# Optimization experiments

Measured on AMD Instinct MI355X. Metric: run time of the kernel, lower is better.

Reference implementation:

```python
import jax, jax.numpy as jnp
import numpy as np

B, S, D_ENC, D_DEC, UNITS = 64, 2048, 512, 512, 512


def setup_inputs() -> dict:
    key = jax.random.key(0)
    ks = jax.random.split(key, 8)
    enc = jax.random.normal(ks[0], (B, S, D_ENC), dtype=jnp.float32)
    dec = jax.random.normal(ks[1], (B, D_DEC), dtype=jnp.float32)
    # Dense params (glorot-ish scale)
    W1 = jax.random.normal(ks[2], (D_ENC, UNITS), dtype=jnp.float32) / np.sqrt(D_ENC)
    b1 = jnp.zeros((UNITS,), dtype=jnp.float32)
    W2 = jax.random.normal(ks[3], (D_DEC, UNITS), dtype=jnp.float32) / np.sqrt(D_DEC)
    b2 = jnp.zeros((UNITS,), dtype=jnp.float32)
    V = jax.random.normal(ks[4], (UNITS, 1), dtype=jnp.float32) / np.sqrt(UNITS)
    bv = jnp.zeros((1,), dtype=jnp.float32)
    return {"encoder_outputs": enc, "decoder_hidden": dec,
            "W1": W1, "b1": b1, "W2": W2, "b2": b2, "V": V, "bv": bv}


def reference(encoder_outputs, decoder_hidden, W1, b1, W2, b2, V, bv):
    # score_features: [B,S,U] = tanh(W1(enc) + W2(dec)[:,None,:])
    proj_enc = jnp.einsum('bsd,du->bsu', encoder_outputs, W1) + b1
    proj_dec = decoder_hidden @ W2 + b2                      # [B,U]
    feat = jnp.tanh(proj_enc + proj_dec[:, None, :])         # [B,S,U]
    score = jnp.einsum('bsu,uo->bso', feat, V) + bv          # [B,S,1]
    attn = jax.nn.softmax(score, axis=1)                     # softmax over seq
    context = jnp.sum(attn * encoder_outputs, axis=1)        # [B,D_enc]
    return context, jnp.squeeze(attn, axis=-1)
```

## Files before the change

kernel.cpp:

```cpp
#include <hip/hip_runtime.h>
#include <hip/hip_bf16.h>

#define BATCH 64
#define SEQ   2048
#define DIM   512
#define MROWS (BATCH * SEQ)

typedef short bf16x8 __attribute__((ext_vector_type(8)));
typedef float f32x4  __attribute__((ext_vector_type(4)));

static __device__ __forceinline__ unsigned short f2bf(float f) {
    union { float f; unsigned u; } v; v.f = f;
    unsigned u = v.u;
    u += 0x7FFFu + ((u >> 16) & 1u);
    return (unsigned short)(u >> 16);
}

static __device__ __forceinline__ float tanh_fast(float x) {
    float xc = fminf(20.0f, fmaxf(-20.0f, x));
#if __has_builtin(__builtin_amdgcn_exp2f)
    float t = __builtin_amdgcn_exp2f(2.885390082f * xc);
#else
    float t = exp2f(2.885390082f * xc);
#endif
#if __has_builtin(__builtin_amdgcn_rcpf)
    return (t - 1.0f) * __builtin_amdgcn_rcpf(t + 1.0f);
#else
    return (t - 1.0f) / (t + 1.0f);
#endif
}

typedef __attribute__((address_space(1))) const unsigned int gu32;
typedef __attribute__((address_space(3))) unsigned int lu32;
static __device__ __forceinline__ void gload_lds16(const unsigned short* g,
                                                   unsigned short* l) {
    __builtin_amdgcn_global_load_lds((gu32*)g, (lu32*)l, 16, 0, 0);
}

__global__ void prep_w1t_kernel(const float* __restrict__ W1,
                                unsigned short* __restrict__ w1t) {
    int stride = gridDim.x * blockDim.x;
    for (int i = blockIdx.x * blockDim.x + threadIdx.x; i < DIM * DIM; i += stride) {
        int k = i >> 9;
        int u = i & 511;
        w1t[u * DIM + k] = f2bf(W1[i]);
    }
}

__global__ void proj_dec_v2(const float* __restrict__ dec,
                            const float* __restrict__ W2,
                            const float* __restrict__ b1,
                            const float* __restrict__ b2,
                            float* __restrict__ pd) {
    __shared__ float sdec[DIM];
    __shared__ float red[4 * 64];
    const int ug = blockIdx.x;
    const int b  = blockIdx.y;
    const int t  = threadIdx.x;
    sdec[t]       = dec[b * DIM + t];
    sdec[t + 256] = dec[b * DIM + t + 256];
    __syncthreads();
    const int u  = ug * 64 + (t & 63);
    const int kq = t >> 6;
    float acc = 0.f;
    #pragma unroll 4
    for (int k = kq * 128; k < kq * 128 + 128; ++k)
        acc += sdec[k] * W2[k * DIM + u];
    red[kq * 64 + (t & 63)] = acc;
    __syncthreads();
    if (t < 64) {
        int u_g = ug * 64 + t;
        float s = red[t] + red[64 + t] + red[128 + t] + red[192 + t]
                + b1[u_g] + b2[u_g];
        pd[b * DIM + u_g] = s;
    }
}

#define BM3 64
#define BK3 64

__global__ __launch_bounds__(256, 2) void gemm_score_v6(
    const float* __restrict__ enc,
    const unsigned short* __restrict__ w1t,
    const float* __restrict__ pd,
    const float* __restrict__ V,
    float* __restrict__ scores,
    float* __restrict__ cnum,
    float* __restrict__ zacc)
{
    __shared__ unsigned short sA[BM3 * BK3];
    __shared__ unsigned short sB[DIM * BK3];

    const int tid  = threadIdx.x;
    const int lane = tid & 63;
    const int wave = tid >> 6;
    const int quad = lane >> 4;
    const int l15  = lane & 15;

    const int row0 = blockIdx.x * BM3;

    f32x4 acc[8][4];
    for (int j = 0; j < 8; ++j)
        for (int tr = 0; tr < 4; ++tr)
            acc[j][tr] = (f32x4){0.f, 0.f, 0.f, 0.f};

    for (int k0 = 0; k0 < DIM; k0 += BK3) {
        for (int i = 0; i < 16; ++i) {
            int c  = i * 256 + tid;
            int r  = c >> 3;
            int cc = c & 7;
            int gc = cc ^ (r & 7);
            gload_lds16(w1t + (size_t)r * DIM + k0 + gc * 8, &sB[c * 8]);
        }
        for (int i = 0; i < 2; ++i) {
            int c  = i * 256 + tid;
            int r  = c >> 3;
            int cc = c & 7;
            const float4* p =
                (const float4*)(enc + (size_t)(row0 + r) * DIM + k0 + cc * 8);
            float4 va = p[0], vb = p[1];
            union { ushort4 s[2]; uint4 q; } o;
            o.s[0].x = f2bf(va.x); o.s[0].y = f2bf(va.y);
            o.s[0].z = f2bf(va.z); o.s[0].w = f2bf(va.w);
            o.s[1].x = f2bf(vb.x); o.s[1].y = f2bf(vb.y);
            o.s[1].z = f2bf(vb.z); o.s[1].w = f2bf(vb.w);
            *(uint4*)(&sA[r * BK3 + ((cc ^ (r & 7)) * 8)]) = o.q;
        }
        __syncthreads();

        for (int kk = 0; kk < BK3; kk += 32) {
            int jc = (kk >> 3) + quad;
            bf16x8 af[4];
            for (int tr = 0; tr < 4; ++tr) {
                int am = tr * 16 + l15;
                af[tr] = *(const bf16x8*)(&sA[am * BK3 + ((jc ^ (am & 7)) * 8)]);
            }
            for (int j = 0; j < 8; ++j) {
                int u = wave * 128 + j * 16 + l15;
                bf16x8 bfr = *(const bf16x8*)(&sB[u * BK3 + ((jc ^ (u & 7)) * 8)]);
                for (int tr = 0; tr < 4; ++tr)
                    acc[j][tr] = __builtin_amdgcn_mfma_f32_16x16x32_bf16(
                        af[tr], bfr, acc[j][tr], 0, 0, 0);
            }
        }
        __syncthreads();
    }

    const int b = row0 >> 11;
    float sacc[4][4];
    for (int tr = 0; tr < 4; ++tr)
        for (int r = 0; r < 4; ++r) sacc[tr][r] = 0.f;

    for (int j = 0; j < 8; ++j) {
        int u_g   = wave * 128 + j * 16 + l15;
        float pdv = pd[b * DIM + u_g];
        float vv  = V[u_g];
        for (int tr = 0; tr < 4; ++tr)
            for (int r = 0; r < 4; ++r)
                sacc[tr][r] += tanh_fast(acc[j][tr][r] + pdv) * vv;
    }
    for (int tr = 0; tr < 4; ++tr)
        for (int r = 0; r < 4; ++r) {
            float v = sacc[tr][r];
            v += __shfl_xor(v, 1);
            v += __shfl_xor(v, 2);
            v += __shfl_xor(v, 4);
            v += __shfl_xor(v, 8);
            sacc[tr][r] = v;
        }
    float* red  = (float*)sA;
    float* eLds = ((float*)sA) + 256;
    if (l15 == 0) {
        for (int tr = 0; tr < 4; ++tr)
            for (int r = 0; r < 4; ++r)
                red[wave * BM3 + tr * 16 + quad * 4 + r] = sacc[tr][r];
    }
    __syncthreads();
    if (tid < BM3) {
        float s = red[tid] + red[BM3 + tid] + red[2 * BM3 + tid] + red[3 * BM3 + tid];
        scores[row0 + tid] = s;
        eLds[tid] = expf(s);
    }
    __syncthreads();

    if (wave == 0) {
        float e = eLds[lane];
        e += __shfl_xor(e, 32);
        e += __shfl_xor(e, 16);
        e += __shfl_xor(e, 8);
        e += __shfl_xor(e, 4);
        e += __shfl_xor(e, 2);
        e += __shfl_xor(e, 1);
        if (lane == 0) atomicAdd(&zacc[b], e);
    }
    {
        const int d = tid * 2;
        const float* ebase = enc + (size_t)row0 * DIM + d;
        float cx = 0.f, cy = 0.f;
        #pragma unroll 4
        for (int r = 0; r < BM3; ++r) {
            float w = eLds[r];
            float2 x = *(const float2*)(ebase + (size_t)r * DIM);
            cx += w * x.x;
            cy += w * x.y;
        }
        atomicAdd(&cnum[b * DIM + d],     cx);
        atomicAdd(&cnum[b * DIM + d + 1], cy);
    }
}

__global__ void finalize_kernel(const float* __restrict__ scores,
                                const float* __restrict__ cnum,
                                const float* __restrict__ zacc,
                                float* __restrict__ attn,
                                float* __restrict__ ctx) {
    const int c = blockIdx.x;
    const int b = blockIdx.y;
    const int t = threadIdx.x;
    const float invZ = 1.0f / zacc[b];
    for (int i = 0; i < 2; ++i) {
        int s = c * 512 + t + i * 256;
        attn[(size_t)b * SEQ + s] = expf(scores[(size_t)b * SEQ + s]) * invZ;
    }
    if (c == 0) {
        ctx[b * DIM + t]       = cnum[b * DIM + t]       * invZ;
        ctx[b * DIM + t + 256] = cnum[b * DIM + t + 256] * invZ;
    }
}

extern "C" void kernel_launch(void* const* d_in, const int* in_sizes, int n_in,
                              void* d_out, int out_size, void* d_ws, size_t ws_size,
                              hipStream_t stream) {
    const float* enc = (const float*)d_in[0];
    const float* dec = (const float*)d_in[1];
    const float* W1  = (const float*)d_in[2];
    const float* b1  = (const float*)d_in[3];
    const float* W2  = (const float*)d_in[4];
    const float* b2  = (const float*)d_in[5];
    const float* V   = (const float*)d_in[6];

    float* out  = (float*)d_out;
    float* ctx  = out;
    float* attn = out + BATCH * DIM;

    char* ws = (char*)d_ws;
    float* pd            = (float*)ws;
    unsigned short* w1t  = (unsigned short*)(ws + 131072);
    float* scores        = (float*)(ws + 131072 + 524288);
    float* cnum          = (float*)(ws + 131072 + 524288 + 524288);
    float* zacc          = (float*)(ws + 131072 + 524288 + 524288 + 131072);

    hipMemsetAsync(cnum, 0, (size_t)BATCH * DIM * 4 + BATCH * 4, stream);

    prep_w1t_kernel<<<256, 256, 0, stream>>>(W1, w1t);
    proj_dec_v2<<<dim3(8, BATCH), 256, 0, stream>>>(dec, W2, b1, b2, pd);
    gemm_score_v6<<<MROWS / BM3, 256, 0, stream>>>(enc, w1t, pd, V, scores,
                                                   cnum, zacc);
    finalize_kernel<<<dim3(4, BATCH), 256, 0, stream>>>(scores, cnum, zacc,
                                                        attn, ctx);
}
```

Before: 448.1 us.

## Double row tile to 128 with 8 waves to amortize W1 tile loads

The fused GEMM+score kernel now processes 128 rows per block with 512 threads arranged as 2x4 waves, so each staged W1 K-slice in LDS is reused across twice as many encoder rows. This halves the global/L2 traffic for W1 per row and halves the number of atomic updates to the context and normalizer accumulators. The epilogue reduction and context accumulation are remapped to the new wave layout. LDS use per block grows, and register pressure under launch_bounds(512,4) may cause spills or lower occupancy.

```diff
diff --git a/kernel.cpp b/kernel.cpp
--- a/kernel.cpp
+++ b/kernel.cpp
@@ -76,10 +76,10 @@
     }
 }
 
-#define BM3 64
-#define BK3 64
-
-__global__ __launch_bounds__(256, 2) void gemm_score_v6(
+#define BM7 128
+#define BK7 64
+
+__global__ __launch_bounds__(512, 4) void gemm_score_v7(
     const float* __restrict__ enc,
     const unsigned short* __restrict__ w1t,
     const float* __restrict__ pd,
@@ -88,32 +88,34 @@
     float* __restrict__ cnum,
     float* __restrict__ zacc)
 {
-    __shared__ unsigned short sA[BM3 * BK3];
-    __shared__ unsigned short sB[DIM * BK3];
+    __shared__ unsigned short sA[BM7 * BK7];
+    __shared__ unsigned short sB[DIM * BK7];
 
     const int tid  = threadIdx.x;
     const int lane = tid & 63;
     const int wave = tid >> 6;
+    const int wm   = wave & 1;
+    const int wn   = wave >> 1;
     const int quad = lane >> 4;
     const int l15  = lane & 15;
 
-    const int row0 = blockIdx.x * BM3;
+    const int row0 = blockIdx.x * BM7;
 
     f32x4 acc[8][4];
     for (int j = 0; j < 8; ++j)
         for (int tr = 0; tr < 4; ++tr)
             acc[j][tr] = (f32x4){0.f, 0.f, 0.f, 0.f};
 
-    for (int k0 = 0; k0 < DIM; k0 += BK3) {
-        for (int i = 0; i < 16; ++i) {
-            int c  = i * 256 + tid;
+    for (int k0 = 0; k0 < DIM; k0 += BK7) {
+        for (int i = 0; i < 8; ++i) {
+            int c  = i * 512 + tid;
             int r  = c >> 3;
             int cc = c & 7;
             int gc = cc ^ (r & 7);
             gload_lds16(w1t + (size_t)r * DIM + k0 + gc * 8, &sB[c * 8]);
         }
         for (int i = 0; i < 2; ++i) {
-            int c  = i * 256 + tid;
+            int c  = i * 512 + tid;
             int r  = c >> 3;
             int cc = c & 7;
             const float4* p =
@@ -124,20 +126,20 @@
             o.s[0].z = f2bf(va.z); o.s[0].w = f2bf(va.w);
             o.s[1].x = f2bf(vb.x); o.s[1].y = f2bf(vb.y);
             o.s[1].z = f2bf(vb.z); o.s[1].w = f2bf(vb.w);
-            *(uint4*)(&sA[r * BK3 + ((cc ^ (r & 7)) * 8)]) = o.q;
+            *(uint4*)(&sA[r * BK7 + ((cc ^ (r & 7)) * 8)]) = o.q;
         }
         __syncthreads();
 
-        for (int kk = 0; kk < BK3; kk += 32) {
+        for (int kk = 0; kk < BK7; kk += 32) {
             int jc = (kk >> 3) + quad;
             bf16x8 af[4];
             for (int tr = 0; tr < 4; ++tr) {
-                int am = tr * 16 + l15;
-                af[tr] = *(const bf16x8*)(&sA[am * BK3 + ((jc ^ (am & 7)) * 8)]);
+                int am = wm * 64 + tr * 16 + l15;
+                af[tr] = *(const bf16x8*)(&sA[am * BK7 + ((jc ^ (am & 7)) * 8)]);
             }
             for (int j = 0; j < 8; ++j) {
-                int u = wave * 128 + j * 16 + l15;
-                bf16x8 bfr = *(const bf16x8*)(&sB[u * BK3 + ((jc ^ (u & 7)) * 8)]);
+                int u = wn * 128 + j * 16 + l15;
+                bf16x8 bfr = *(const bf16x8*)(&sB[u * BK7 + ((jc ^ (u & 7)) * 8)]);
                 for (int tr = 0; tr < 4; ++tr)
                     acc[j][tr] = __builtin_amdgcn_mfma_f32_16x16x32_bf16(
                         af[tr], bfr, acc[j][tr], 0, 0, 0);
@@ -152,7 +154,7 @@
         for (int r = 0; r < 4; ++r) sacc[tr][r] = 0.f;
 
     for (int j = 0; j < 8; ++j) {
-        int u_g   = wave * 128 + j * 16 + l15;
+        int u_g   = wn * 128 + j * 16 + l15;
         float pdv = pd[b * DIM + u_g];
         float vv  = V[u_g];
         for (int tr = 0; tr < 4; ++tr)
@@ -169,22 +171,25 @@
             sacc[tr][r] = v;
         }
     float* red  = (float*)sA;
-    float* eLds = ((float*)sA) + 256;
+    float* eLds = ((float*)sA) + 512;
     if (l15 == 0) {
         for (int tr = 0; tr < 4; ++tr)
             for (int r = 0; r < 4; ++r)
-                red[wave * BM3 + tr * 16 + quad * 4 + r] = sacc[tr][r];
-    }
-    __syncthreads();
-    if (tid < BM3) {
-        float s = red[tid] + red[BM3 + tid] + red[2 * BM3 + tid] + red[3 * BM3 + tid];
+                red[wave * 64 + tr * 16 + quad * 4 + r] = sacc[tr][r];
+    }
+    __syncthreads();
+    if (tid < BM7) {
+        int m  = tid >> 6;
+        int lr = tid & 63;
+        float s = red[(0 * 2 + m) * 64 + lr] + red[(1 * 2 + m) * 64 + lr]
+                + red[(2 * 2 + m) * 64 + lr] + red[(3 * 2 + m) * 64 + lr];
         scores[row0 + tid] = s;
         eLds[tid] = expf(s);
     }
     __syncthreads();
 
-    if (wave == 0) {
-        float e = eLds[lane];
+    if (wave < 2) {
+        float e = eLds[wave * 64 + lane];
         e += __shfl_xor(e, 32);
         e += __shfl_xor(e, 16);
         e += __shfl_xor(e, 8);
@@ -194,18 +199,12 @@
         if (lane == 0) atomicAdd(&zacc[b], e);
     }
     {
-        const int d = tid * 2;
-        const float* ebase = enc + (size_t)row0 * DIM + d;
-        float cx = 0.f, cy = 0.f;
+        const float* ebase = enc + (size_t)row0 * DIM + tid;
+        float cx = 0.f;
         #pragma unroll 4
-        for (int r = 0; r < BM3; ++r) {
-            float w = eLds[r];
-            float2 x = *(const float2*)(ebase + (size_t)r * DIM);
-            cx += w * x.x;
-            cy += w * x.y;
-        }
-        atomicAdd(&cnum[b * DIM + d],     cx);
-        atomicAdd(&cnum[b * DIM + d + 1], cy);
+        for (int r = 0; r < BM7; ++r)
+            cx += eLds[r] * ebase[(size_t)r * DIM];
+        atomicAdd(&cnum[b * DIM + tid], cx);
     }
 }
 
@@ -254,7 +253,7 @@
 
     prep_w1t_kernel<<<256, 256, 0, stream>>>(W1, w1t);
     proj_dec_v2<<<dim3(8, BATCH), 256, 0, stream>>>(dec, W2, b1, b2, pd);
-    gemm_score_v6<<<MROWS / BM3, 256, 0, stream>>>(enc, w1t, pd, V, scores,
+    gemm_score_v7<<<MROWS / BM7, 512, 0, stream>>>(enc, w1t, pd, V, scores,
                                                    cnum, zacc);
     finalize_kernel<<<dim3(4, BATCH), 256, 0, stream>>>(scores, cnum, zacc,
                                                         attn, ctx);
```

Result: slower. 844.2 us (+88.4%).
